# Optimization experiments

Hardware: AMD Instinct MI355X
Metric: run time of the kernel (lower is better)

## Reference

```python
import jax, jax.numpy as jnp
import numpy as np

N_QUBITS = 13
DEPTH = 4
DIM = 2 ** N_QUBITS
PI = 3.141592653589793

# qubit 0 = most significant bit of the basis-state index
_idx = np.arange(DIM)
BITS = np.stack([(_idx >> (N_QUBITS - 1 - q)) & 1 for q in range(N_QUBITS)], axis=1)  # (DIM, n)
SIGNS = jnp.asarray(1.0 - 2.0 * BITS, dtype=jnp.float32)                               # Z eigenvalues, (DIM, n)
PARITY = jnp.asarray((-1.0) ** BITS.sum(axis=1), dtype=jnp.float32)                    # <Z^{(x)n}> diagonal, (DIM,)
# CZ entangling chain (q, q+1): diagonal (-1)^{sum_q b_q b_{q+1}}
ENT = jnp.asarray((-1.0) ** (BITS[:, :-1] * BITS[:, 1:]).sum(axis=1), dtype=jnp.float32)


def fwht(psi):
    """Normalized fast Walsh-Hadamard transform (H on every qubit), psi: (B, DIM) complex."""
    B = psi.shape[0]
    for q in range(N_QUBITS):
        psi = psi.reshape(B, 2 ** q, 2, -1)
        psi = jnp.stack([psi[:, :, 0] + psi[:, :, 1], psi[:, :, 0] - psi[:, :, 1]], axis=2)
    return psi.reshape(B, DIM) * (2.0 ** (-N_QUBITS / 2))


def feature_map_state(x):
    """Havlicek ZZ feature map: psi = D(x) H^n D(x) H^n |0...0>.
    Diagonal phase per basis state b: sum_j x_j s_j(b) + sum_{j<k} (pi-x_j)(pi-x_k) s_j(b) s_k(b)."""
    a = PI - x                                              # (B, n)
    u = x @ SIGNS.T                                         # (B, DIM)
    v = a @ SIGNS.T                                         # (B, DIM)
    phi = u + 0.5 * (v * v - jnp.sum(a * a, axis=1, keepdims=True))  # pair term via (sum)^2 trick
    d = jnp.exp(1j * phi)                                   # complex64 diagonal
    psi = jnp.full((x.shape[0], DIM), DIM ** -0.5, dtype=jnp.complex64)  # H^n |0>
    psi = fwht(d * psi)
    return d * psi


def _apply_1q(psi, U, q):
    """Apply 2x2 complex gate U to qubit q (bit-sliced)."""
    B = psi.shape[0]
    psi = psi.reshape(B, 2 ** q, 2, -1)
    a0, a1 = psi[:, :, 0], psi[:, :, 1]
    out = jnp.stack([U[0, 0] * a0 + U[0, 1] * a1, U[1, 0] * a0 + U[1, 1] * a1], axis=2)
    return out.reshape(B, DIM)


def variational_apply(psi, theta):
    """(DEPTH+1) layers of per-qubit Rz(b)Ry(a), CZ-chain entanglers between layers."""
    th = theta.reshape(DEPTH + 1, N_QUBITS, 2)
    for l in range(DEPTH + 1):
        if l > 0:
            psi = psi * ENT
        for q in range(N_QUBITS):
            ca = jnp.cos(0.5 * th[l, q, 0])
            sa = jnp.sin(0.5 * th[l, q, 0])
            em = jnp.exp(-0.5j * th[l, q, 1])
            ep = jnp.exp(0.5j * th[l, q, 1])
            U = jnp.stack([jnp.stack([em * ca, -em * sa]), jnp.stack([ep * sa, ep * ca])])
            psi = _apply_1q(psi, U, q)
    return psi


def setup_inputs() -> dict:
    key = jax.random.key(0)
    k1, k2 = jax.random.split(key)
    x = jax.random.normal(k1, (512, N_QUBITS), dtype=jnp.float32)
    theta = 0.1 * jax.random.normal(k2, ((DEPTH + 1) * N_QUBITS * 2,), dtype=jnp.float32)
    bias = jnp.zeros((1,), dtype=jnp.float32)
    return {"x": x, "theta": theta, "bias": bias}


def reference(x, theta, bias):
    psi = feature_map_state(x)
    psi = variational_apply(psi, theta)
    prob = psi.real ** 2 + psi.imag ** 2              # (B, DIM)
    logit = prob @ PARITY + bias[0]                   # (B,)
    return jnp.stack([-logit, logit], axis=1)         # two-class logits
```

## Files before the change

kernel.cpp:

```cpp
#include <hip/hip_runtime.h>
#include <hip/hip_fp16.h>

#define NQ   13
#define DIM  8192
#define PI_F 3.14159265358979323846f
#define NT   512
#define NAMP 16

#define NSLOT 9216

__device__ __forceinline__ int baseA(int t) { return 16 * t + 4 * (t >> 1); }
__device__ __forceinline__ int baseB(int t, int g) {
  int m = t & 31;
  return 4 * m + 4 * (m >> 3) + 144 * ((t >> 6) & 7) + 1152 * ((t >> 5) & 1) + 2304 * g;
}

union F4H { float4 f; __half2 h[4]; };

__device__ __forceinline__ void rsincos(float x, float* s, float* c) {
  const float INV2PI = 0.15915494309189535f;
  const float TWOPI  = 6.283185307179586f;
  float r = x * INV2PI;
  r -= rintf(r);
  float ang = r * TWOPI;
  *s = __sinf(ang);
  *c = __cosf(ang);
}

__device__ __forceinline__ float2 f2fma(float s, float2 a, float2 b) {
  return make_float2(fmaf(s, a.x, b.x), fmaf(s, a.y, b.y));
}
__device__ __forceinline__ float2 f2add(float2 a, float2 b) {
  return make_float2(a.x + b.x, a.y + b.y);
}
__device__ __forceinline__ float2 f2sub(float2 a, float2 b) {
  return make_float2(a.x - b.x, a.y - b.y);
}
__device__ __forceinline__ float2 cphase(float2 v, float cs, float sn) {
  return make_float2(fmaf(cs, v.x, -sn * v.y), fmaf(cs, v.y, sn * v.x));
}
__device__ __forceinline__ float2 cmul(float2 a, float2 b) {
  return make_float2(fmaf(a.x, b.x, -a.y * b.y), fmaf(a.x, b.y, a.y * b.x));
}

template<int MASK>
__device__ __forceinline__ int xorLaneI(int x) {
  if constexpr (MASK == 1)
    return __builtin_amdgcn_update_dpp(x, x, 0xB1, 0xF, 0xF, false);
  else if constexpr (MASK == 2)
    return __builtin_amdgcn_update_dpp(x, x, 0x4E, 0xF, 0xF, false);
  else
    return __shfl_xor(x, MASK, 64);
}
template<int MASK>
__device__ __forceinline__ __half2 xorLaneH(__half2 v) {
  union { __half2 h; int i; } u; u.h = v;
  u.i = xorLaneI<MASK>(u.i);
  return u.h;
}
template<int MASK>
__device__ __forceinline__ float xorLaneF(float v) {
  union { float f; int i; } u; u.f = v;
  u.i = xorLaneI<MASK>(u.i);
  return u.f;
}

__device__ __forceinline__ void loadAh(const __half2* __restrict__ sAmp, int t, __half2* amp) {
  const __half2* p = sAmp + baseA(t);
  #pragma unroll
  for (int k = 0; k < 4; k++) {
    F4H u; u.f = *reinterpret_cast<const float4*>(p + 4 * k);
    #pragma unroll
    for (int c = 0; c < 4; c++) amp[4 * k + c] = u.h[c];
  }
}
__device__ __forceinline__ void storeAh(__half2* __restrict__ sAmp, int t, const __half2* amp) {
  __half2* p = sAmp + baseA(t);
  #pragma unroll
  for (int k = 0; k < 4; k++) {
    F4H u;
    #pragma unroll
    for (int c = 0; c < 4; c++) u.h[c] = amp[4 * k + c];
    *reinterpret_cast<float4*>(p + 4 * k) = u.f;
  }
}
__device__ __forceinline__ void loadBh(const __half2* __restrict__ sAmp, int t, __half2* amp) {
  #pragma unroll
  for (int g = 0; g < 4; g++) {
    F4H u; u.f = *reinterpret_cast<const float4*>(sAmp + baseB(t, g));
    #pragma unroll
    for (int c = 0; c < 4; c++) amp[4 * g + c] = u.h[c];
  }
}
__device__ __forceinline__ void storeBh(__half2* __restrict__ sAmp, int t, const __half2* amp) {
  #pragma unroll
  for (int g = 0; g < 4; g++) {
    F4H u;
    #pragma unroll
    for (int c = 0; c < 4; c++) u.h[c] = amp[4 * g + c];
    *reinterpret_cast<float4*>(sAmp + baseB(t, g)) = u.f;
  }
}

template<int KB>
__device__ __forceinline__ void fwht_bit(float2* amp) {
  #pragma unroll
  for (int j = 0; j < NAMP; j++) if (!(j & (1 << KB))) {
    int j1 = j | (1 << KB);
    float2 a0 = amp[j], a1 = amp[j1];
    amp[j]  = f2add(a0, a1);
    amp[j1] = f2sub(a0, a1);
  }
}
template<int KB>
__device__ __forceinline__ void applyRy(float2* amp, float ta, float sa) {
  #pragma unroll
  for (int j = 0; j < NAMP; j++) if (!(j & (1 << KB))) {
    int j1 = j | (1 << KB);
    amp[j]  = f2fma(-ta, amp[j1], amp[j]);
    amp[j1] = f2fma( sa, amp[j],  amp[j1]);
    amp[j]  = f2fma(-ta, amp[j1], amp[j]);
  }
}

template<int MASK>
__device__ __forceinline__ void laneRyH(__half2* amp, __half2 c2, __half2 spm) {
  #pragma unroll
  for (int j = 0; j < NAMP; j++) {
    __half2 p = xorLaneH<MASK>(amp[j]);
    amp[j] = __hfma2(spm, p, __hmul2(c2, amp[j]));
  }
}
template<int MASK>
__device__ __forceinline__ void laneFwhtH(__half2* amp, __half2 sgn) {
  #pragma unroll
  for (int j = 0; j < NAMP; j++) {
    __half2 p = xorLaneH<MASK>(amp[j]);
    amp[j] = __hfma2(sgn, amp[j], p);
  }
}
template<int MASK>
__device__ __forceinline__ void laneFwhtF(float2* amp, float sgn) {
  #pragma unroll
  for (int j = 0; j < NAMP; j++) {
    float px = xorLaneF<MASK>(amp[j].x);
    float py = xorLaneF<MASK>(amp[j].y);
    amp[j].x = fmaf(sgn, amp[j].x, px);
    amp[j].y = fmaf(sgn, amp[j].y, py);
  }
}

template<int PAT>
__device__ __forceinline__ void buildTree(const float* __restrict__ w, float bias,
                                          int t, float* s) {
  float base = bias;
  if constexpr (PAT == 0) {
    #pragma unroll
    for (int k = 0; k < 9; k++) base += ((t >> k) & 1) ? w[4 + k] : 0.0f;
  } else {
    constexpr int BM[9] = {2, 3, 4, 5, 6, 10, 7, 8, 9};
    #pragma unroll
    for (int k = 0; k < 9; k++) base += ((t >> k) & 1) ? w[BM[k]] : 0.0f;
  }
  constexpr int PA[4] = {0, 1, 2, 3};
  constexpr int PB[4] = {0, 1, 11, 12};
  s[0] = base;
  #pragma unroll
  for (int k = 0; k < 4; k++) {
    float wp = w[(PAT == 0) ? PA[k] : PB[k]];
    #pragma unroll
    for (int m = 0; m < (1 << k); m++) s[m | (1 << k)] = s[m] + wp;
  }
}

template<int PAT, bool INIT>
__device__ __forceinline__ void featureDiag(float2* amp,
                                            const float* __restrict__ wX,
                                            const float* __restrict__ wA,
                                            const float* __restrict__ cons, int t) {
  float u[NAMP], v[NAMP];
  buildTree<PAT>(wX, cons[0], t, u);
  buildTree<PAT>(wA, cons[1], t, v);
  float A2 = cons[2];
  #pragma unroll
  for (int j = 0; j < NAMP; j++) {
    float phi = u[j] + 0.5f * (v[j] * v[j] - A2);
    float sn, cs; rsincos(phi, &sn, &cs);
    if constexpr (INIT) amp[j] = make_float2(cs, sn);
    else                amp[j] = cphase(amp[j], cs, sn);
  }
}

__device__ __forceinline__ void applyDiagA(float2* amp,
                                           const float* __restrict__ wb,
                                           const float* __restrict__ eR,
                                           const float* __restrict__ eI,
                                           float bias, int t) {
  float base = bias;
  #pragma unroll
  for (int k = 0; k < 9; k++) base += ((t >> k) & 1) ? wb[4 + k] : 0.0f;
  float2 c[16];
  { float sn, cs; rsincos(base, &sn, &cs); c[0] = make_float2(cs, sn); }
  #pragma unroll
  for (int k = 0; k < 4; k++) {
    float2 e = make_float2(eR[k], eI[k]);
    #pragma unroll
    for (int m = 0; m < (1 << k); m++) c[m | (1 << k)] = cmul(c[m], e);
  }
  int st = __popc(t & (t >> 1)) & 1;
  int tb = t & 1;
  #pragma unroll
  for (int j = 0; j < 16; j++) {
    int sgb = st ^ (((j >> 3) & tb)) ^ (__popc(j & (j >> 1)) & 1);
    float sgn = sgb ? -1.0f : 1.0f;
    amp[j] = cphase(amp[j], c[j].x * sgn, c[j].y * sgn);
  }
}

__global__ __launch_bounds__(NT, 4) void qc_kernel(
    const float* __restrict__ xin,
    const float* __restrict__ thin,
    const float* __restrict__ bin,
    float* __restrict__ out) {
  __shared__ alignas(16) __half2 sAmp[NSLOT];
  __shared__ float gTA[65], gSA[65];
  __shared__ __half2 hC2[65], hS2[65];
  __shared__ float gBbit[65];
  __shared__ float eBr[65], eBi[65];
  __shared__ float wX[13], wA[13];
  __shared__ float cons[8];
  __shared__ float red[NT / 64];

  const int t = threadIdx.x;
  const int lane = t & 63;
  const int b = blockIdx.x;

  if (t < NQ) {
    float xq = xin[b * NQ + t];
    float aq = PI_F - xq;
    wX[12 - t] = -2.0f * xq;
    wA[12 - t] = -2.0f * aq;
  }
  if (t < 65) {
    float av = thin[2 * t];
    float bv = thin[2 * t + 1];
    float ca = cosf(0.5f * av);
    float sa = sinf(0.5f * av);
    float ta = sa / (1.0f + ca);
    gTA[t] = ta;
    gSA[t] = sa;
    hC2[t] = __float2half2_rn(ca);
    hS2[t] = __float2half2_rn(sa);
    int l = t / NQ, q = t % NQ;
    int s = l * NQ + (12 - q);
    gBbit[s] = bv;
    eBr[s] = cosf(bv);
    eBi[s] = sinf(bv);
  }
  __syncthreads();
  if (t == 0) {
    float X = 0.f, A = 0.f, A2 = 0.f;
    for (int p = 0; p < NQ; p++) {
      float xq = -0.5f * wX[p], aq = -0.5f * wA[p];
      X += xq; A += aq; A2 += aq * aq;
    }
    cons[0] = X; cons[1] = A; cons[2] = A2;
    for (int l = 0; l < 5; l++) {
      float s = 0.f;
      for (int p = 0; p < NQ; p++) s += gBbit[l * NQ + p];
      cons[3 + l] = -0.5f * s;
    }
  }
  __syncthreads();

  {
    float2 amp[NAMP];
    featureDiag<0, true>(amp, wX, wA, cons, t);
    fwht_bit<0>(amp); fwht_bit<1>(amp); fwht_bit<2>(amp); fwht_bit<3>(amp);
    laneFwhtF<1>(amp, (lane & 1) ? -1.0f : 1.0f);
    __half2 h[NAMP];
    #pragma unroll
    for (int j = 0; j < NAMP; j++) h[j] = __float22half2_rn(amp[j]);
    const __half2 P1 = __float2half2_rn(1.0f), M1 = __float2half2_rn(-1.0f);
    laneFwhtH<2>(h,  (lane & 2)  ? M1 : P1);
    laneFwhtH<4>(h,  (lane & 4)  ? M1 : P1);
    laneFwhtH<8>(h,  (lane & 8)  ? M1 : P1);
    laneFwhtH<16>(h, (lane & 16) ? M1 : P1);
    laneFwhtH<32>(h, (lane & 32) ? M1 : P1);
    storeAh(sAmp, t, h);
  }
  __syncthreads();

  {
    __half2 h[NAMP];
    loadBh(sAmp, t, h);
    float2 amp[NAMP];
    #pragma unroll
    for (int j = 0; j < NAMP; j++) amp[j] = __half22float2(h[j]);
    laneFwhtF<32>(amp, (lane & 32) ? -1.0f : 1.0f);
    fwht_bit<2>(amp); fwht_bit<3>(amp);
    featureDiag<1, false>(amp, wX, wA, cons, t);
    applyRy<2>(amp, gTA[1], gSA[1]);
    applyRy<3>(amp, gTA[0], gSA[0]);
    #pragma unroll
    for (int j = 0; j < NAMP; j++) h[j] = __float22half2_rn(amp[j]);
    __half2 s2 = hS2[2];
    __half2 spm = (lane & 32) ? s2 : __hneg2(s2);
    laneRyH<32>(h, hC2[2], spm);
    storeBh(sAmp, t, h);
  }
  __syncthreads();

  float acc = 0.0f;
  for (int l = 0; l < 5; l++) {
    const int g = l * NQ;
    {
      __half2 h[NAMP];
      loadAh(sAmp, t, h);
      {
        __half2 s2, spm;
        s2 = hS2[g + 8]; spm = (lane & 1)  ? s2 : __hneg2(s2); laneRyH<1>(h,  hC2[g + 8], spm);
        s2 = hS2[g + 7]; spm = (lane & 2)  ? s2 : __hneg2(s2); laneRyH<2>(h,  hC2[g + 7], spm);
        s2 = hS2[g + 6]; spm = (lane & 4)  ? s2 : __hneg2(s2); laneRyH<4>(h,  hC2[g + 6], spm);
        s2 = hS2[g + 5]; spm = (lane & 8)  ? s2 : __hneg2(s2); laneRyH<8>(h,  hC2[g + 5], spm);
        s2 = hS2[g + 4]; spm = (lane & 16) ? s2 : __hneg2(s2); laneRyH<16>(h, hC2[g + 4], spm);
        s2 = hS2[g + 3]; spm = (lane & 32) ? s2 : __hneg2(s2); laneRyH<32>(h, hC2[g + 3], spm);
      }
      float2 amp[NAMP];
      #pragma unroll
      for (int j = 0; j < NAMP; j++) amp[j] = __half22float2(h[j]);
      applyRy<0>(amp, gTA[g + 12], gSA[g + 12]);
      applyRy<1>(amp, gTA[g + 11], gSA[g + 11]);
      applyRy<2>(amp, gTA[g + 10], gSA[g + 10]);
      applyRy<3>(amp, gTA[g + 9],  gSA[g + 9]);
      if (l < 4) {
        applyDiagA(amp, gBbit + g, eBr + g, eBi + g, cons[3 + l], t);
        #pragma unroll
        for (int j = 0; j < NAMP; j++) h[j] = __float22half2_rn(amp[j]);
        storeAh(sAmp, t, h);
      } else {
        int pt = __popc(t) & 1;
        #pragma unroll
        for (int j = 0; j < NAMP; j++) {
          float p2 = fmaf(amp[j].x, amp[j].x, amp[j].y * amp[j].y);
          acc += ((pt + __popc(j)) & 1) ? -p2 : p2;
        }
      }
    }
    if (l < 4) {
      __syncthreads();
      const int g1 = g + NQ;
      {
        __half2 h[NAMP];
        loadBh(sAmp, t, h);
        __half2 s2 = hS2[g1 + 2];
        __half2 spm = (lane & 32) ? s2 : __hneg2(s2);
        laneRyH<32>(h, hC2[g1 + 2], spm);
        float2 amp[NAMP];
        #pragma unroll
        for (int j = 0; j < NAMP; j++) amp[j] = __half22float2(h[j]);
        applyRy<2>(amp, gTA[g1 + 1], gSA[g1 + 1]);
        applyRy<3>(amp, gTA[g1 + 0], gSA[g1 + 0]);
        #pragma unroll
        for (int j = 0; j < NAMP; j++) h[j] = __float22half2_rn(amp[j]);
        storeBh(sAmp, t, h);
      }
      __syncthreads();
    }
  }

  #pragma unroll
  for (int off = 32; off > 0; off >>= 1) acc += __shfl_down(acc, off, 64);
  if ((t & 63) == 0) red[t >> 6] = acc;
  __syncthreads();
  if (t == 0) {
    float total = 0.f;
    #pragma unroll
    for (int w = 0; w < NT / 64; w++) total += red[w];
    float logit = total * (1.0f / 67108864.0f) + bin[0];
    out[b * 2 + 0] = -logit;
    out[b * 2 + 1] = logit;
  }
}

extern "C" void kernel_launch(void* const* d_in, const int* in_sizes, int n_in,
                              void* d_out, int out_size, void* d_ws, size_t ws_size,
                              hipStream_t stream) {
  const float* x  = (const float*)d_in[0];
  const float* th = (const float*)d_in[1];
  const float* bi = (const float*)d_in[2];
  float* out = (float*)d_out;
  int B = in_sizes[0] / NQ;
  qc_kernel<<<B, NT, 0, stream>>>(x, th, bi, out);
}
```

Before: 102.5 us.

## Restructure statevector kernel to 256 threads with 32 amplitudes each

Halves the threads per block and doubles the amplitudes held per thread. The work is split into two layouts, one covering the high 8 qubits per thread and one with a strided low layout, so five qubits are handled in registers and only two need DPP lane exchanges. Cross-lane __shfl_xor is gone, layers are fused in pairs so each pair needs fewer LDS round trips and barriers, and more Ry gates run in packed half precision. The cost is higher register pressure (launch bounds drop to 1 block minimum), more half-precision rounding error, and a strided LDS access pattern that could cause bank conflicts.

After: 91.23 us. -11.0%, faster.

```diff
diff --git a/kernel.cpp b/kernel.cpp
--- a/kernel.cpp
+++ b/kernel.cpp
@@ -4,15 +4,15 @@
 #define NQ   13
 #define DIM  8192
 #define PI_F 3.14159265358979323846f
-#define NT   512
-#define NAMP 16
+#define NT   256
+#define NAMP 32
 
 #define NSLOT 9216
 
-__device__ __forceinline__ int baseA(int t) { return 16 * t + 4 * (t >> 1); }
-__device__ __forceinline__ int baseB(int t, int g) {
-  int m = t & 31;
-  return 4 * m + 4 * (m >> 3) + 144 * ((t >> 6) & 7) + 1152 * ((t >> 5) & 1) + 2304 * g;
+__device__ __forceinline__ int baseH(int t) { return 36 * t; }
+__device__ __forceinline__ int baseL(int t) {
+  int c = ((t & 1) << 7) | ((t & 2) << 5) | (t >> 2);
+  return c + 4 * (c >> 5);
 }
 
 union F4H { float4 f; __half2 h[4]; };
@@ -47,10 +47,8 @@
 __device__ __forceinline__ int xorLaneI(int x) {
   if constexpr (MASK == 1)
     return __builtin_amdgcn_update_dpp(x, x, 0xB1, 0xF, 0xF, false);
-  else if constexpr (MASK == 2)
+  else
     return __builtin_amdgcn_update_dpp(x, x, 0x4E, 0xF, 0xF, false);
-  else
-    return __shfl_xor(x, MASK, 64);
 }
 template<int MASK>
 __device__ __forceinline__ __half2 xorLaneH(__half2 v) {
@@ -58,48 +56,35 @@
   u.i = xorLaneI<MASK>(u.i);
   return u.h;
 }
-template<int MASK>
-__device__ __forceinline__ float xorLaneF(float v) {
-  union { float f; int i; } u; u.f = v;
-  u.i = xorLaneI<MASK>(u.i);
-  return u.f;
-}
-
-__device__ __forceinline__ void loadAh(const __half2* __restrict__ sAmp, int t, __half2* amp) {
-  const __half2* p = sAmp + baseA(t);
-  #pragma unroll
-  for (int k = 0; k < 4; k++) {
+
+__device__ __forceinline__ void loadHh(const __half2* __restrict__ sAmp, int t, __half2* amp) {
+  const __half2* p = sAmp + baseH(t);
+  #pragma unroll
+  for (int k = 0; k < 8; k++) {
     F4H u; u.f = *reinterpret_cast<const float4*>(p + 4 * k);
     #pragma unroll
     for (int c = 0; c < 4; c++) amp[4 * k + c] = u.h[c];
   }
 }
-__device__ __forceinline__ void storeAh(__half2* __restrict__ sAmp, int t, const __half2* amp) {
-  __half2* p = sAmp + baseA(t);
-  #pragma unroll
-  for (int k = 0; k < 4; k++) {
+__device__ __forceinline__ void storeHh(__half2* __restrict__ sAmp, int t, const __half2* amp) {
+  __half2* p = sAmp + baseH(t);
+  #pragma unroll
+  for (int k = 0; k < 8; k++) {
     F4H u;
     #pragma unroll
     for (int c = 0; c < 4; c++) u.h[c] = amp[4 * k + c];
     *reinterpret_cast<float4*>(p + 4 * k) = u.f;
   }
 }
-__device__ __forceinline__ void loadBh(const __half2* __restrict__ sAmp, int t, __half2* amp) {
-  #pragma unroll
-  for (int g = 0; g < 4; g++) {
-    F4H u; u.f = *reinterpret_cast<const float4*>(sAmp + baseB(t, g));
-    #pragma unroll
-    for (int c = 0; c < 4; c++) amp[4 * g + c] = u.h[c];
-  }
-}
-__device__ __forceinline__ void storeBh(__half2* __restrict__ sAmp, int t, const __half2* amp) {
-  #pragma unroll
-  for (int g = 0; g < 4; g++) {
-    F4H u;
-    #pragma unroll
-    for (int c = 0; c < 4; c++) u.h[c] = amp[4 * g + c];
-    *reinterpret_cast<float4*>(sAmp + baseB(t, g)) = u.f;
-  }
+__device__ __forceinline__ void loadLh(const __half2* __restrict__ sAmp, int t, __half2* amp) {
+  const __half2* p = sAmp + baseL(t);
+  #pragma unroll
+  for (int j = 0; j < NAMP; j++) amp[j] = p[288 * j];
+}
+__device__ __forceinline__ void storeLh(__half2* __restrict__ sAmp, int t, const __half2* amp) {
+  __half2* p = sAmp + baseL(t);
+  #pragma unroll
+  for (int j = 0; j < NAMP; j++) p[288 * j] = amp[j];
 }
 
 template<int KB>
@@ -123,6 +108,17 @@
   }
 }
 
+template<int KB>
+__device__ __forceinline__ void applyRyH(__half2* amp, __half2 nta, __half2 sa) {
+  #pragma unroll
+  for (int j = 0; j < NAMP; j++) if (!(j & (1 << KB))) {
+    int j1 = j | (1 << KB);
+    amp[j]  = __hfma2(nta, amp[j1], amp[j]);
+    amp[j1] = __hfma2(sa,  amp[j],  amp[j1]);
+    amp[j]  = __hfma2(nta, amp[j1], amp[j]);
+  }
+}
+
 template<int MASK>
 __device__ __forceinline__ void laneRyH(__half2* amp, __half2 c2, __half2 spm) {
   #pragma unroll
@@ -137,16 +133,6 @@
   for (int j = 0; j < NAMP; j++) {
     __half2 p = xorLaneH<MASK>(amp[j]);
     amp[j] = __hfma2(sgn, amp[j], p);
-  }
-}
-template<int MASK>
-__device__ __forceinline__ void laneFwhtF(float2* amp, float sgn) {
-  #pragma unroll
-  for (int j = 0; j < NAMP; j++) {
-    float px = xorLaneF<MASK>(amp[j].x);
-    float py = xorLaneF<MASK>(amp[j].y);
-    amp[j].x = fmaf(sgn, amp[j].x, px);
-    amp[j].y = fmaf(sgn, amp[j].y, py);
   }
 }
 
@@ -156,18 +142,18 @@
   float base = bias;
   if constexpr (PAT == 0) {
     #pragma unroll
-    for (int k = 0; k < 9; k++) base += ((t >> k) & 1) ? w[4 + k] : 0.0f;
+    for (int k = 0; k < 8; k++) base += ((t >> k) & 1) ? w[5 + k] : 0.0f;
   } else {
-    constexpr int BM[9] = {2, 3, 4, 5, 6, 10, 7, 8, 9};
-    #pragma unroll
-    for (int k = 0; k < 9; k++) base += ((t >> k) & 1) ? w[BM[k]] : 0.0f;
-  }
-  constexpr int PA[4] = {0, 1, 2, 3};
-  constexpr int PB[4] = {0, 1, 11, 12};
+    constexpr int BM[8] = {7, 6, 0, 1, 2, 3, 4, 5};
+    #pragma unroll
+    for (int k = 0; k < 8; k++) base += ((t >> k) & 1) ? w[BM[k]] : 0.0f;
+  }
+  constexpr int PH[5] = {0, 1, 2, 3, 4};
+  constexpr int PL[5] = {8, 9, 10, 11, 12};
   s[0] = base;
   #pragma unroll
-  for (int k = 0; k < 4; k++) {
-    float wp = w[(PAT == 0) ? PA[k] : PB[k]];
+  for (int k = 0; k < 5; k++) {
+    float wp = w[(PAT == 0) ? PH[k] : PL[k]];
     #pragma unroll
     for (int m = 0; m < (1 << k); m++) s[m | (1 << k)] = s[m] + wp;
   }
@@ -175,13 +161,13 @@
 
 template<int PAT, bool INIT>
 __device__ __forceinline__ void featureDiag(float2* amp,
-                                            const float* __restrict__ wX,
-                                            const float* __restrict__ wA,
-                                            const float* __restrict__ cons, int t) {
+                                            const float* __restrict__ wXp,
+                                            const float* __restrict__ wAp,
+                                            const float* __restrict__ consp, int t) {
   float u[NAMP], v[NAMP];
-  buildTree<PAT>(wX, cons[0], t, u);
-  buildTree<PAT>(wA, cons[1], t, v);
-  float A2 = cons[2];
+  buildTree<PAT>(wXp, consp[0], t, u);
+  buildTree<PAT>(wAp, consp[1], t, v);
+  float A2 = consp[2];
   #pragma unroll
   for (int j = 0; j < NAMP; j++) {
     float phi = u[j] + 0.5f * (v[j] * v[j] - A2);
@@ -191,39 +177,55 @@
   }
 }
 
-__device__ __forceinline__ void applyDiagA(float2* amp,
-                                           const float* __restrict__ wb,
-                                           const float* __restrict__ eR,
-                                           const float* __restrict__ eI,
-                                           float bias, int t) {
+template<int PAT>
+__device__ __forceinline__ void applyDiag(float2* amp,
+                                          const float* __restrict__ wb,
+                                          const float* __restrict__ eR,
+                                          const float* __restrict__ eI,
+                                          float bias, int t) {
   float base = bias;
-  #pragma unroll
-  for (int k = 0; k < 9; k++) base += ((t >> k) & 1) ? wb[4 + k] : 0.0f;
+  if constexpr (PAT == 0) {
+    #pragma unroll
+    for (int k = 0; k < 8; k++) base += ((t >> k) & 1) ? wb[5 + k] : 0.0f;
+  } else {
+    constexpr int BM[8] = {7, 6, 0, 1, 2, 3, 4, 5};
+    #pragma unroll
+    for (int k = 0; k < 8; k++) base += ((t >> k) & 1) ? wb[BM[k]] : 0.0f;
+  }
+  constexpr int E0 = (PAT == 0) ? 0 : 8;
+  const int ct = (PAT == 0) ? 0 : (((t & 1) << 7) | ((t & 2) << 5) | (t >> 2));
   float2 c[16];
   { float sn, cs; rsincos(base, &sn, &cs); c[0] = make_float2(cs, sn); }
   #pragma unroll
   for (int k = 0; k < 4; k++) {
-    float2 e = make_float2(eR[k], eI[k]);
+    float2 e = make_float2(eR[E0 + k], eI[E0 + k]);
     #pragma unroll
     for (int m = 0; m < (1 << k); m++) c[m | (1 << k)] = cmul(c[m], e);
   }
-  int st = __popc(t & (t >> 1)) & 1;
-  int tb = t & 1;
   #pragma unroll
   for (int j = 0; j < 16; j++) {
-    int sgb = st ^ (((j >> 3) & tb)) ^ (__popc(j & (j >> 1)) & 1);
-    float sgn = sgb ? -1.0f : 1.0f;
+    int i = (PAT == 0) ? ((t << 5) | j) : ((j << 8) | ct);
+    float sgn = (__popc(i & (i >> 1)) & 1) ? -1.0f : 1.0f;
     amp[j] = cphase(amp[j], c[j].x * sgn, c[j].y * sgn);
   }
-}
-
-__global__ __launch_bounds__(NT, 4) void qc_kernel(
+  float2 e4 = make_float2(eR[E0 + 4], eI[E0 + 4]);
+  #pragma unroll
+  for (int j = 16; j < 32; j++) {
+    int i = (PAT == 0) ? ((t << 5) | j) : ((j << 8) | ct);
+    float sgn = (__popc(i & (i >> 1)) & 1) ? -1.0f : 1.0f;
+    float2 cc = cmul(c[j - 16], e4);
+    amp[j] = cphase(amp[j], cc.x * sgn, cc.y * sgn);
+  }
+}
+
+__global__ __launch_bounds__(NT, 1) void qc_kernel(
     const float* __restrict__ xin,
     const float* __restrict__ thin,
     const float* __restrict__ bin,
     float* __restrict__ out) {
   __shared__ alignas(16) __half2 sAmp[NSLOT];
   __shared__ float gTA[65], gSA[65];
+  __shared__ __half2 hNTA[65], hSA[65];
   __shared__ __half2 hC2[65], hS2[65];
   __shared__ float gBbit[65];
   __shared__ float eBr[65], eBi[65];
@@ -249,8 +251,10 @@
     float ta = sa / (1.0f + ca);
     gTA[t] = ta;
     gSA[t] = sa;
-    hC2[t] = __float2half2_rn(ca);
-    hS2[t] = __float2half2_rn(sa);
+    hNTA[t] = __float2half2_rn(-ta);
+    hSA[t]  = __float2half2_rn(sa);
+    hC2[t]  = __float2half2_rn(ca);
+    hS2[t]  = __float2half2_rn(sa);
     int l = t / NQ, q = t % NQ;
     int s = l * NQ + (12 - q);
     gBbit[s] = bv;
@@ -273,99 +277,127 @@
   }
   __syncthreads();
 
+  const __half2 P1 = __float2half2_rn(1.0f), M1 = __float2half2_rn(-1.0f);
+
   {
-    float2 amp[NAMP];
-    featureDiag<0, true>(amp, wX, wA, cons, t);
-    fwht_bit<0>(amp); fwht_bit<1>(amp); fwht_bit<2>(amp); fwht_bit<3>(amp);
-    laneFwhtF<1>(amp, (lane & 1) ? -1.0f : 1.0f);
-    __half2 h[NAMP];
-    #pragma unroll
-    for (int j = 0; j < NAMP; j++) h[j] = __float22half2_rn(amp[j]);
-    const __half2 P1 = __float2half2_rn(1.0f), M1 = __float2half2_rn(-1.0f);
-    laneFwhtH<2>(h,  (lane & 2)  ? M1 : P1);
-    laneFwhtH<4>(h,  (lane & 4)  ? M1 : P1);
-    laneFwhtH<8>(h,  (lane & 8)  ? M1 : P1);
-    laneFwhtH<16>(h, (lane & 16) ? M1 : P1);
-    laneFwhtH<32>(h, (lane & 32) ? M1 : P1);
-    storeAh(sAmp, t, h);
+    float2 ampF[NAMP];
+    featureDiag<0, true>(ampF, wX, wA, cons, t);
+    fwht_bit<0>(ampF); fwht_bit<1>(ampF); fwht_bit<2>(ampF);
+    fwht_bit<3>(ampF); fwht_bit<4>(ampF);
+    __half2 ampH[NAMP];
+    #pragma unroll
+    for (int j = 0; j < NAMP; j++) ampH[j] = __float22half2_rn(ampF[j]);
+    laneFwhtH<1>(ampH, (lane & 1) ? M1 : P1);
+    laneFwhtH<2>(ampH, (lane & 2) ? M1 : P1);
+    storeHh(sAmp, t, ampH);
   }
   __syncthreads();
 
   {
-    __half2 h[NAMP];
-    loadBh(sAmp, t, h);
-    float2 amp[NAMP];
-    #pragma unroll
-    for (int j = 0; j < NAMP; j++) amp[j] = __half22float2(h[j]);
-    laneFwhtF<32>(amp, (lane & 32) ? -1.0f : 1.0f);
-    fwht_bit<2>(amp); fwht_bit<3>(amp);
-    featureDiag<1, false>(amp, wX, wA, cons, t);
-    applyRy<2>(amp, gTA[1], gSA[1]);
-    applyRy<3>(amp, gTA[0], gSA[0]);
-    #pragma unroll
-    for (int j = 0; j < NAMP; j++) h[j] = __float22half2_rn(amp[j]);
-    __half2 s2 = hS2[2];
-    __half2 spm = (lane & 32) ? s2 : __hneg2(s2);
-    laneRyH<32>(h, hC2[2], spm);
-    storeBh(sAmp, t, h);
+    __half2 ampH[NAMP];
+    loadLh(sAmp, t, ampH);
+    laneFwhtH<1>(ampH, (lane & 1) ? M1 : P1);
+    float2 ampF[NAMP];
+    #pragma unroll
+    for (int j = 0; j < NAMP; j++) ampF[j] = __half22float2(ampH[j]);
+    fwht_bit<0>(ampF); fwht_bit<1>(ampF); fwht_bit<2>(ampF);
+    fwht_bit<3>(ampF); fwht_bit<4>(ampF);
+    featureDiag<1, false>(ampF, wX, wA, cons, t);
+    applyRy<2>(ampF, gTA[2], gSA[2]);
+    applyRy<3>(ampF, gTA[1], gSA[1]);
+    applyRy<4>(ampF, gTA[0], gSA[0]);
+    #pragma unroll
+    for (int j = 0; j < NAMP; j++) ampH[j] = __float22half2_rn(ampF[j]);
+    applyRyH<0>(ampH, hNTA[4], hSA[4]);
+    applyRyH<1>(ampH, hNTA[3], hSA[3]);
+    { __half2 s2 = hS2[5];
+      laneRyH<1>(ampH, hC2[5], (lane & 1) ? s2 : __hneg2(s2)); }
+    storeLh(sAmp, t, ampH);
   }
   __syncthreads();
 
+  for (int l = 0; l < 4; l += 2) {
+    const int g = l * NQ, g1 = g + NQ, g2 = g1 + NQ;
+    {
+      __half2 ampH[NAMP];
+      loadHh(sAmp, t, ampH);
+      { __half2 s2 = hS2[g + 7];
+        laneRyH<1>(ampH, hC2[g + 7], (lane & 1) ? s2 : __hneg2(s2)); }
+      { __half2 s2 = hS2[g + 6];
+        laneRyH<2>(ampH, hC2[g + 6], (lane & 2) ? s2 : __hneg2(s2)); }
+      applyRyH<2>(ampH, hNTA[g + 10], hSA[g + 10]);
+      applyRyH<3>(ampH, hNTA[g + 9],  hSA[g + 9]);
+      applyRyH<4>(ampH, hNTA[g + 8],  hSA[g + 8]);
+      float2 ampF[NAMP];
+      #pragma unroll
+      for (int j = 0; j < NAMP; j++) ampF[j] = __half22float2(ampH[j]);
+      applyRy<0>(ampF, gTA[g + 12], gSA[g + 12]);
+      applyRy<1>(ampF, gTA[g + 11], gSA[g + 11]);
+      applyDiag<0>(ampF, gBbit + g, eBr + g, eBi + g, cons[3 + l], t);
+      applyRy<0>(ampF, gTA[g1 + 12], gSA[g1 + 12]);
+      applyRy<1>(ampF, gTA[g1 + 11], gSA[g1 + 11]);
+      #pragma unroll
+      for (int j = 0; j < NAMP; j++) ampH[j] = __float22half2_rn(ampF[j]);
+      applyRyH<2>(ampH, hNTA[g1 + 10], hSA[g1 + 10]);
+      applyRyH<3>(ampH, hNTA[g1 + 9],  hSA[g1 + 9]);
+      applyRyH<4>(ampH, hNTA[g1 + 8],  hSA[g1 + 8]);
+      { __half2 s2 = hS2[g1 + 7];
+        laneRyH<1>(ampH, hC2[g1 + 7], (lane & 1) ? s2 : __hneg2(s2)); }
+      { __half2 s2 = hS2[g1 + 6];
+        laneRyH<2>(ampH, hC2[g1 + 6], (lane & 2) ? s2 : __hneg2(s2)); }
+      storeHh(sAmp, t, ampH);
+    }
+    __syncthreads();
+    {
+      __half2 ampH[NAMP];
+      loadLh(sAmp, t, ampH);
+      { __half2 s2 = hS2[g1 + 5];
+        laneRyH<1>(ampH, hC2[g1 + 5], (lane & 1) ? s2 : __hneg2(s2)); }
+      applyRyH<0>(ampH, hNTA[g1 + 4], hSA[g1 + 4]);
+      applyRyH<1>(ampH, hNTA[g1 + 3], hSA[g1 + 3]);
+      float2 ampF[NAMP];
+      #pragma unroll
+      for (int j = 0; j < NAMP; j++) ampF[j] = __half22float2(ampH[j]);
+      applyRy<2>(ampF, gTA[g1 + 2], gSA[g1 + 2]);
+      applyRy<3>(ampF, gTA[g1 + 1], gSA[g1 + 1]);
+      applyRy<4>(ampF, gTA[g1 + 0], gSA[g1 + 0]);
+      applyDiag<1>(ampF, gBbit + g1, eBr + g1, eBi + g1, cons[3 + l + 1], t);
+      applyRy<2>(ampF, gTA[g2 + 2], gSA[g2 + 2]);
+      applyRy<3>(ampF, gTA[g2 + 1], gSA[g2 + 1]);
+      applyRy<4>(ampF, gTA[g2 + 0], gSA[g2 + 0]);
+      #pragma unroll
+      for (int j = 0; j < NAMP; j++) ampH[j] = __float22half2_rn(ampF[j]);
+      applyRyH<0>(ampH, hNTA[g2 + 4], hSA[g2 + 4]);
+      applyRyH<1>(ampH, hNTA[g2 + 3], hSA[g2 + 3]);
+      { __half2 s2 = hS2[g2 + 5];
+        laneRyH<1>(ampH, hC2[g2 + 5], (lane & 1) ? s2 : __hneg2(s2)); }
+      storeLh(sAmp, t, ampH);
+    }
+    __syncthreads();
+  }
+
   float acc = 0.0f;
-  for (int l = 0; l < 5; l++) {
-    const int g = l * NQ;
-    {
-      __half2 h[NAMP];
-      loadAh(sAmp, t, h);
-      {
-        __half2 s2, spm;
-        s2 = hS2[g + 8]; spm = (lane & 1)  ? s2 : __hneg2(s2); laneRyH<1>(h,  hC2[g + 8], spm);
-        s2 = hS2[g + 7]; spm = (lane & 2)  ? s2 : __hneg2(s2); laneRyH<2>(h,  hC2[g + 7], spm);
-        s2 = hS2[g + 6]; spm = (lane & 4)  ? s2 : __hneg2(s2); laneRyH<4>(h,  hC2[g + 6], spm);
-        s2 = hS2[g + 5]; spm = (lane & 8)  ? s2 : __hneg2(s2); laneRyH<8>(h,  hC2[g + 5], spm);
-        s2 = hS2[g + 4]; spm = (lane & 16) ? s2 : __hneg2(s2); laneRyH<16>(h, hC2[g + 4], spm);
-        s2 = hS2[g + 3]; spm = (lane & 32) ? s2 : __hneg2(s2); laneRyH<32>(h, hC2[g + 3], spm);
-      }
-      float2 amp[NAMP];
-      #pragma unroll
-      for (int j = 0; j < NAMP; j++) amp[j] = __half22float2(h[j]);
-      applyRy<0>(amp, gTA[g + 12], gSA[g + 12]);
-      applyRy<1>(amp, gTA[g + 11], gSA[g + 11]);
-      applyRy<2>(amp, gTA[g + 10], gSA[g + 10]);
-      applyRy<3>(amp, gTA[g + 9],  gSA[g + 9]);
-      if (l < 4) {
-        applyDiagA(amp, gBbit + g, eBr + g, eBi + g, cons[3 + l], t);
-        #pragma unroll
-        for (int j = 0; j < NAMP; j++) h[j] = __float22half2_rn(amp[j]);
-        storeAh(sAmp, t, h);
-      } else {
-        int pt = __popc(t) & 1;
-        #pragma unroll
-        for (int j = 0; j < NAMP; j++) {
-          float p2 = fmaf(amp[j].x, amp[j].x, amp[j].y * amp[j].y);
-          acc += ((pt + __popc(j)) & 1) ? -p2 : p2;
-        }
-      }
-    }
-    if (l < 4) {
-      __syncthreads();
-      const int g1 = g + NQ;
-      {
-        __half2 h[NAMP];
-        loadBh(sAmp, t, h);
-        __half2 s2 = hS2[g1 + 2];
-        __half2 spm = (lane & 32) ? s2 : __hneg2(s2);
-        laneRyH<32>(h, hC2[g1 + 2], spm);
-        float2 amp[NAMP];
-        #pragma unroll
-        for (int j = 0; j < NAMP; j++) amp[j] = __half22float2(h[j]);
-        applyRy<2>(amp, gTA[g1 + 1], gSA[g1 + 1]);
-        applyRy<3>(amp, gTA[g1 + 0], gSA[g1 + 0]);
-        #pragma unroll
-        for (int j = 0; j < NAMP; j++) h[j] = __float22half2_rn(amp[j]);
-        storeBh(sAmp, t, h);
-      }
-      __syncthreads();
+  {
+    const int g = 4 * NQ;
+    __half2 ampH[NAMP];
+    loadHh(sAmp, t, ampH);
+    { __half2 s2 = hS2[g + 7];
+      laneRyH<1>(ampH, hC2[g + 7], (lane & 1) ? s2 : __hneg2(s2)); }
+    { __half2 s2 = hS2[g + 6];
+      laneRyH<2>(ampH, hC2[g + 6], (lane & 2) ? s2 : __hneg2(s2)); }
+    applyRyH<2>(ampH, hNTA[g + 10], hSA[g + 10]);
+    applyRyH<3>(ampH, hNTA[g + 9],  hSA[g + 9]);
+    applyRyH<4>(ampH, hNTA[g + 8],  hSA[g + 8]);
+    float2 ampF[NAMP];
+    #pragma unroll
+    for (int j = 0; j < NAMP; j++) ampF[j] = __half22float2(ampH[j]);
+    applyRy<0>(ampF, gTA[g + 12], gSA[g + 12]);
+    applyRy<1>(ampF, gTA[g + 11], gSA[g + 11]);
+    int pt = __popc(t) & 1;
+    #pragma unroll
+    for (int j = 0; j < NAMP; j++) {
+      float p2 = fmaf(ampF[j].x, ampF[j].x, ampF[j].y * ampF[j].y);
+      acc += ((pt + __popc(j)) & 1) ? -p2 : p2;
     }
   }
 
@@ -374,9 +406,7 @@
   if ((t & 63) == 0) red[t >> 6] = acc;
   __syncthreads();
   if (t == 0) {
-    float total = 0.f;
-    #pragma unroll
-    for (int w = 0; w < NT / 64; w++) total += red[w];
+    float total = red[0] + red[1] + red[2] + red[3];
     float logit = total * (1.0f / 67108864.0f) + bin[0];
     out[b * 2 + 0] = -logit;
     out[b * 2 + 1] = logit;
```
